# Performance work log

Measured on AMD Instinct MI355X. Metric: run time of the kernel, lower is better.

Reference implementation:

```python
import jax, jax.numpy as jnp
import numpy as np

B, D_IN, D_OUT, Q, NUM_CLASSES = 256, 512, 256, 16, 100
POOL = 2  # patch_size = sqrt(n=4) -> 2x2 spatial mean pooling


def setup_inputs() -> dict:
    key = jax.random.key(0)
    k1, k2, k3 = jax.random.split(key, 3)
    X = jax.random.normal(k1, (B, D_IN, Q), jnp.float32)
    # FRMap weight init: randn(d_out, d_in) / sqrt(d_in)
    W = jax.random.normal(k2, (D_OUT, D_IN), jnp.float32) / np.sqrt(D_IN)
    d2 = D_OUT // POOL
    fc_w = jax.random.normal(k3, (NUM_CLASSES, d2 * d2), jnp.float32) / np.sqrt(d2 * d2)
    fc_b = jnp.zeros((NUM_CLASSES,), jnp.float32)
    return {"X": X, "W": W, "fc_w": fc_w, "fc_b": fc_b}


def reference(X, W, fc_w, fc_b):
    # FRMap: Y = W @ X  -> (B, d_out, q)
    Y = jnp.einsum('oi,biq->boq', W, X)
    # ReOrth: Q from reduced QR of Y -> orthonormal (B, d_out, q)
    Qm, _ = jnp.linalg.qr(Y)
    # ProjMap: P = Q Q^T -> (B, d_out, d_out)
    P = jnp.einsum('biq,bjq->bij', Qm, Qm)
    # ProjPooling (spatial, n=4): 2x2 mean pooling == adaptive_avg_pool2d to (d/2, d/2)
    b, d, _ = P.shape
    d2 = d // POOL
    Pp = P.reshape(b, d2, POOL, d2, POOL).mean(axis=(2, 4))  # (B, d2, d2)
    # OrthMap: top-q eigenvectors of symmetric Pp (eigh ascending -> take last q, descending)
    _, V = jnp.linalg.eigh(Pp)
    U = V[..., ::-1][..., :Q]  # (B, d2, q)
    # OutputBlock: ProjMap + flatten + FC
    P2 = jnp.einsum('biq,bjq->bij', U, U)  # (B, d2, d2)
    logits = P2.reshape(b, -1) @ fc_w.T + fc_b  # (B, num_classes)
    return logits
```

## Files before the change

kernel.cpp:

```cpp
#include <hip/hip_runtime.h>
#include <hip/hip_bf16.h>
#include <cstdint>

#define BATCH 256
#define DIN   512
#define D2    128
#define NQ    16
#define NC    100
#define KFC   (D2 * D2)

#define KS    32
#define KCH   (KFC / KS)
#define STEPS (KCH / 32)

#define ZPAD  132
#define XTP   520
#define CVT_BLKS 800
#define W2_BLKS  256

typedef short short8 __attribute__((ext_vector_type(8)));
typedef float f32x4  __attribute__((ext_vector_type(4)));
typedef float f32x16 __attribute__((ext_vector_type(16)));

__global__ __launch_bounds__(256) void k_prep(const float* __restrict__ W,
                                              const float* __restrict__ fcw,
                                              __hip_bfloat16* __restrict__ W2hi,
                                              __hip_bfloat16* __restrict__ W2lo,
                                              __hip_bfloat16* __restrict__ fcw16) {
    int blk = blockIdx.x;
    if (blk < CVT_BLKS) {
        int i = (blk * 256 + threadIdx.x) * 8;
        float4 a = *(const float4*)(fcw + i);
        float4 b = *(const float4*)(fcw + i + 4);
        short8 v;
        __hip_bfloat16* h = (__hip_bfloat16*)&v;
        h[0] = __float2bfloat16(a.x); h[1] = __float2bfloat16(a.y);
        h[2] = __float2bfloat16(a.z); h[3] = __float2bfloat16(a.w);
        h[4] = __float2bfloat16(b.x); h[5] = __float2bfloat16(b.y);
        h[6] = __float2bfloat16(b.z); h[7] = __float2bfloat16(b.w);
        *(short8*)(fcw16 + i) = v;
    } else {
        int idx = (blk - CVT_BLKS) * 256 + threadIdx.x;
        int o = idx >> 9;
        int i = idx & (DIN - 1);
        float v = 0.5f * (W[(size_t)(2 * o) * DIN + i] +
                          W[(size_t)(2 * o + 1) * DIN + i]);
        __hip_bfloat16 hi = __float2bfloat16(v);
        __hip_bfloat16 lo = __float2bfloat16(v - __bfloat162float(hi));
        W2hi[idx] = hi;
        W2lo[idx] = lo;
    }
}

#define GJ_STEP(K) do {                                                   \
    float piv = __shfl(g[(K) & 7], ((K) >> 3) * 16 + (K), 64);            \
    float fac = __shfl(g[(K) & 7], ((K) >> 3) * 16 + r, 64);              \
    float inv = 1.0f / piv;                                               \
    float f   = fac * inv;                                                \
    float p0 = __shfl(g[0], cg16 + (K), 64);                              \
    float p1 = __shfl(g[1], cg16 + (K), 64);                              \
    float p2 = __shfl(g[2], cg16 + (K), 64);                              \
    float p3 = __shfl(g[3], cg16 + (K), 64);                              \
    float p4 = __shfl(g[4], cg16 + (K), 64);                              \
    float p5 = __shfl(g[5], cg16 + (K), 64);                              \
    float p6 = __shfl(g[6], cg16 + (K), 64);                              \
    float p7 = __shfl(g[7], cg16 + (K), 64);                              \
    bool isk = (r == (K));                                                \
    g[0] = isk ? p0 * inv : fmaf(-f, p0, g[0]);                           \
    g[1] = isk ? p1 * inv : fmaf(-f, p1, g[1]);                           \
    g[2] = isk ? p2 * inv : fmaf(-f, p2, g[2]);                           \
    g[3] = isk ? p3 * inv : fmaf(-f, p3, g[3]);                           \
    g[4] = isk ? p4 * inv : fmaf(-f, p4, g[4]);                           \
    g[5] = isk ? p5 * inv : fmaf(-f, p5, g[5]);                           \
    g[6] = isk ? p6 * inv : fmaf(-f, p6, g[6]);                           \
    g[7] = isk ? p7 * inv : fmaf(-f, p7, g[7]);                           \
} while (0)

__global__ __launch_bounds__(512) void k_zgep(const float* __restrict__ X,
                                              const __hip_bfloat16* __restrict__ W2hi,
                                              const __hip_bfloat16* __restrict__ W2lo,
                                              __hip_bfloat16* __restrict__ P2) {
    __shared__ float Xs[DIN][17];
    __shared__ __hip_bfloat16 Xthi[NQ][XTP];
    __shared__ __hip_bfloat16 Xtlo[NQ][XTP];
    __shared__ float Zt[NQ][ZPAD];
    __shared__ float Et[NQ][ZPAD];
    __shared__ float Gi[NQ][36];

    int b = blockIdx.x;
    int t = threadIdx.x;
    int l = t & 63;
    int wv = t >> 6;

    {
        const float4* src = (const float4*)(X + (size_t)b * DIN * NQ);
        #pragma unroll
        for (int r = 0; r < 4; ++r) {
            float4 v = src[t + r * 512];
            int idx = (t + r * 512) * 4;
            int i = idx >> 4, q = idx & 15;
            Xs[i][q]     = v.x;
            Xs[i][q + 1] = v.y;
            Xs[i][q + 2] = v.z;
            Xs[i][q + 3] = v.w;
        }
    }
    __syncthreads();

    {
        int q  = t >> 5;
        int li = t & 31;
        #pragma unroll
        for (int c = 0; c < 8; ++c) {
            int i0 = c * 64 + li * 2;
            float v0 = Xs[i0][q], v1 = Xs[i0 + 1][q];
            __hip_bfloat16 h0 = __float2bfloat16(v0);
            __hip_bfloat16 h1 = __float2bfloat16(v1);
            __hip_bfloat16 l0 = __float2bfloat16(v0 - __bfloat162float(h0));
            __hip_bfloat16 l1 = __float2bfloat16(v1 - __bfloat162float(h1));
            Xthi[q][i0] = h0; Xthi[q][i0 + 1] = h1;
            Xtlo[q][i0] = l0; Xtlo[q][i0 + 1] = l1;
        }
    }
    __syncthreads();

    {
        int m  = l & 15;
        int kg = (l >> 4) * 8;
        const __hip_bfloat16* whi = W2hi + (size_t)(wv * 16 + m) * DIN + kg;
        const __hip_bfloat16* wlo = W2lo + (size_t)(wv * 16 + m) * DIN + kg;
        f32x4 acc = {0.f, 0.f, 0.f, 0.f};
        #pragma unroll 4
        for (int s = 0; s < 16; ++s) {
            short8 ahi = *(const short8*)(whi + s * 32);
            short8 alo = *(const short8*)(wlo + s * 32);
            short8 bhi = *(const short8*)&Xthi[m][s * 32 + kg];
            short8 blo = *(const short8*)&Xtlo[m][s * 32 + kg];
            acc = __builtin_amdgcn_mfma_f32_16x16x32_bf16(ahi, bhi, acc, 0, 0, 0);
            acc = __builtin_amdgcn_mfma_f32_16x16x32_bf16(ahi, blo, acc, 0, 0, 0);
            acc = __builtin_amdgcn_mfma_f32_16x16x32_bf16(alo, bhi, acc, 0, 0, 0);
        }
        int r0 = (l >> 4) * 4;
        #pragma unroll
        for (int j = 0; j < 4; ++j)
            Zt[m][wv * 16 + r0 + j] = acc[j];
    }
    __syncthreads();

    if (t < 256) {
        int qq = t >> 4, rr = t & 15;
        float s = 0.f;
        for (int i = 0; i < D2; i += 4) {
            float4 a = *(const float4*)&Zt[qq][i];
            float4 c = *(const float4*)&Zt[rr][i];
            s = fmaf(a.x, c.x, s); s = fmaf(a.y, c.y, s);
            s = fmaf(a.z, c.z, s); s = fmaf(a.w, c.w, s);
        }
        Gi[qq][rr] = s;
        Gi[qq][NQ + rr] = (qq == rr) ? 1.f : 0.f;
    }
    __syncthreads();

    if (t < 64) {
        int r    = t & 15;
        int cg   = t >> 4;
        int cg16 = cg * 16;
        float g[8];
        #pragma unroll
        for (int j = 0; j < 8; ++j) g[j] = Gi[r][cg * 8 + j];
        GJ_STEP(0);  GJ_STEP(1);  GJ_STEP(2);  GJ_STEP(3);
        GJ_STEP(4);  GJ_STEP(5);  GJ_STEP(6);  GJ_STEP(7);
        GJ_STEP(8);  GJ_STEP(9);  GJ_STEP(10); GJ_STEP(11);
        GJ_STEP(12); GJ_STEP(13); GJ_STEP(14); GJ_STEP(15);
        if (cg >= 2) {
            #pragma unroll
            for (int j = 0; j < 8; ++j) Gi[r][cg * 8 + j] = g[j];
        }
    }
    __syncthreads();

    {
        int o  = t & (D2 - 1);
        int qg = (t >> 7) * 4;
        float acc[4] = {};
        #pragma unroll
        for (int rp = 0; rp < NQ; ++rp) {
            float z = Zt[rp][o];
            #pragma unroll
            for (int j = 0; j < 4; ++j)
                acc[j] = fmaf(z, Gi[rp][NQ + qg + j], acc[j]);
        }
        #pragma unroll
        for (int j = 0; j < 4; ++j) Et[qg + j][o] = acc[j];
    }
    __syncthreads();

    {
        __hip_bfloat16* P2b = P2 + (size_t)b * KFC;
        int ti = wv >> 1;
        int tj0 = (wv & 1) * 2;
        int r8 = (l >> 5) * 8;
        int rm = l & 31;

        short8 afr;
        {
            __hip_bfloat16* ah = (__hip_bfloat16*)&afr;
            #pragma unroll
            for (int j = 0; j < 8; ++j)
                ah[j] = __float2bfloat16(Et[r8 + j][ti * 32 + rm]);
        }
        #pragma unroll
        for (int tjo = 0; tjo < 2; ++tjo) {
            int tj = tj0 + tjo;
            short8 bfr;
            __hip_bfloat16* bh = (__hip_bfloat16*)&bfr;
            #pragma unroll
            for (int j = 0; j < 8; ++j)
                bh[j] = __float2bfloat16(Zt[r8 + j][tj * 32 + rm]);
            f32x16 cc = {};
            cc = __builtin_amdgcn_mfma_f32_32x32x16_bf16(afr, bfr, cc, 0, 0, 0);
            #pragma unroll
            for (int reg = 0; reg < 16; ++reg) {
                int row = (reg & 3) + 8 * (reg >> 2) + 4 * (l >> 5);
                P2b[(size_t)(ti * 32 + row) * D2 + tj * 32 + rm] =
                    __float2bfloat16(cc[reg]);
            }
        }
    }
}

__global__ __launch_bounds__(256) void k_fc(const __hip_bfloat16* __restrict__ P2,
                                            const __hip_bfloat16* __restrict__ fcw16,
                                            float* __restrict__ part) {
    int bt = blockIdx.x;
    int ks = blockIdx.y;
    int t  = threadIdx.x;
    int lane = t & 63;
    int w    = t >> 6;
    int m  = lane & 15;
    int kg = (lane >> 4) * 8;

    const __hip_bfloat16* pa =
        P2 + (size_t)(bt * 16 + m) * KFC + ks * KCH + kg;

    int c0 = w * 32 + m;
    int c1 = c0 + 16;
    bool v0 = (c0 < NC), v1 = (c1 < NC);
    const __hip_bfloat16* pb0 =
        fcw16 + (size_t)(v0 ? c0 : 0) * KFC + ks * KCH + kg;
    const __hip_bfloat16* pb1 =
        fcw16 + (size_t)(v1 ? c1 : 0) * KFC + ks * KCH + kg;

    f32x4 acc0 = {0.f, 0.f, 0.f, 0.f};
    f32x4 acc1 = {0.f, 0.f, 0.f, 0.f};
    short8 zz = {};

    #pragma unroll 4
    for (int s = 0; s < STEPS; ++s) {
        short8 a  = *(const short8*)(pa + s * 32);
        short8 b0 = v0 ? *(const short8*)(pb0 + s * 32) : zz;
        short8 b1 = v1 ? *(const short8*)(pb1 + s * 32) : zz;
        acc0 = __builtin_amdgcn_mfma_f32_16x16x32_bf16(a, b0, acc0, 0, 0, 0);
        acc1 = __builtin_amdgcn_mfma_f32_16x16x32_bf16(a, b1, acc1, 0, 0, 0);
    }

    int r0 = (lane >> 4) * 4;
    float* pp = part + ((size_t)ks * BATCH + bt * 16 + r0) * D2;
    #pragma unroll
    for (int j = 0; j < 4; ++j) {
        pp[(size_t)j * D2 + w * 32 + m]      = acc0[j];
        pp[(size_t)j * D2 + w * 32 + 16 + m] = acc1[j];
    }
}

__global__ __launch_bounds__(128) void k_red(const float* __restrict__ part,
                                             const float* __restrict__ fcb,
                                             float* __restrict__ out) {
    int b = blockIdx.x;
    int c = threadIdx.x;
    if (c < NC) {
        float s = fcb[c];
        #pragma unroll 8
        for (int ks = 0; ks < KS; ++ks)
            s += part[((size_t)ks * BATCH + b) * D2 + c];
        out[(size_t)b * NC + c] = s;
    }
}

extern "C" void kernel_launch(void* const* d_in, const int* in_sizes, int n_in,
                              void* d_out, int out_size, void* d_ws, size_t ws_size,
                              hipStream_t stream) {
    const float* X   = (const float*)d_in[0];
    const float* W   = (const float*)d_in[1];
    const float* fcw = (const float*)d_in[2];
    const float* fcb = (const float*)d_in[3];
    float* out = (float*)d_out;

    __hip_bfloat16* W2hi  = (__hip_bfloat16*)d_ws;
    __hip_bfloat16* W2lo  = W2hi + 65536;
    __hip_bfloat16* fcw16 = W2lo + 65536;
    __hip_bfloat16* P2b16 = fcw16 + 1638400;
    float*          part  = (float*)(P2b16 + 4194304);

    k_prep<<<dim3(CVT_BLKS + W2_BLKS), 256, 0, stream>>>(W, fcw, W2hi, W2lo, fcw16);
    k_zgep<<<dim3(BATCH), 512, 0, stream>>>(X, W2hi, W2lo, P2b16);
    k_fc  <<<dim3(16, KS), 256, 0, stream>>>(P2b16, fcw16, part);
    k_red <<<dim3(BATCH), 128, 0, stream>>>(part, fcb, out);
}
```

Measured before the change: 41.45 us.

## Fuse split-K reduction into FC kernel and pre-swizzle X fragments in LDS

Removes the separate reduction kernel. Each FC block now increments a per-batch-tile atomic counter, and the last of the split-K blocks sums the partial results and adds the bias. The X hi/lo bf16 split is written directly in MFMA fragment order, so each lane loads its operand from LDS contiguously, and bf16 conversion uses a manual round-to-nearest bit trick. This saves one kernel launch plus one global round trip, at the cost of a counter reset in the prep kernel and a serialized tail reduction on the last-arriving block.

Result: slower. 104.0 us (+150.9%).

```diff
diff --git a/kernel.cpp b/kernel.cpp
--- a/kernel.cpp
+++ b/kernel.cpp
@@ -14,19 +14,27 @@
 #define STEPS (KCH / 32)
 
 #define ZPAD  132
-#define XTP   520
 #define CVT_BLKS 800
 #define W2_BLKS  256
 
 typedef short short8 __attribute__((ext_vector_type(8)));
 typedef float f32x4  __attribute__((ext_vector_type(4)));
 typedef float f32x16 __attribute__((ext_vector_type(16)));
+
+static __device__ __forceinline__ unsigned short f2bf_rne(float f) {
+    unsigned x = __float_as_uint(f);
+    return (unsigned short)((x + 0x7fffu + ((x >> 16) & 1u)) >> 16);
+}
+static __device__ __forceinline__ float bf2f(unsigned short u) {
+    return __uint_as_float(((unsigned)u) << 16);
+}
 
 __global__ __launch_bounds__(256) void k_prep(const float* __restrict__ W,
                                               const float* __restrict__ fcw,
                                               __hip_bfloat16* __restrict__ W2hi,
                                               __hip_bfloat16* __restrict__ W2lo,
-                                              __hip_bfloat16* __restrict__ fcw16) {
+                                              __hip_bfloat16* __restrict__ fcw16,
+                                              int* __restrict__ cnt) {
     int blk = blockIdx.x;
     if (blk < CVT_BLKS) {
         int i = (blk * 256 + threadIdx.x) * 8;
@@ -40,15 +48,16 @@
         h[6] = __float2bfloat16(b.z); h[7] = __float2bfloat16(b.w);
         *(short8*)(fcw16 + i) = v;
     } else {
+        if (blk == CVT_BLKS && threadIdx.x < 16) cnt[threadIdx.x] = 0;
         int idx = (blk - CVT_BLKS) * 256 + threadIdx.x;
         int o = idx >> 9;
         int i = idx & (DIN - 1);
         float v = 0.5f * (W[(size_t)(2 * o) * DIN + i] +
                           W[(size_t)(2 * o + 1) * DIN + i]);
-        __hip_bfloat16 hi = __float2bfloat16(v);
-        __hip_bfloat16 lo = __float2bfloat16(v - __bfloat162float(hi));
-        W2hi[idx] = hi;
-        W2lo[idx] = lo;
+        unsigned short hi = f2bf_rne(v);
+        unsigned short lo = f2bf_rne(v - bf2f(hi));
+        *(unsigned short*)(W2hi + idx) = hi;
+        *(unsigned short*)(W2lo + idx) = lo;
     }
 }
 
@@ -81,8 +90,8 @@
                                               const __hip_bfloat16* __restrict__ W2lo,
                                               __hip_bfloat16* __restrict__ P2) {
     __shared__ float Xs[DIN][17];
-    __shared__ __hip_bfloat16 Xthi[NQ][XTP];
-    __shared__ __hip_bfloat16 Xtlo[NQ][XTP];
+    __shared__ unsigned int FragHi[16 * 256];
+    __shared__ unsigned int FragLo[16 * 256];
     __shared__ float Zt[NQ][ZPAD];
     __shared__ float Et[NQ][ZPAD];
     __shared__ float Gi[NQ][36];
@@ -107,20 +116,20 @@
     }
     __syncthreads();
 
-    {
-        int q  = t >> 5;
-        int li = t & 31;
-        #pragma unroll
-        for (int c = 0; c < 8; ++c) {
-            int i0 = c * 64 + li * 2;
-            float v0 = Xs[i0][q], v1 = Xs[i0 + 1][q];
-            __hip_bfloat16 h0 = __float2bfloat16(v0);
-            __hip_bfloat16 h1 = __float2bfloat16(v1);
-            __hip_bfloat16 l0 = __float2bfloat16(v0 - __bfloat162float(h0));
-            __hip_bfloat16 l1 = __float2bfloat16(v1 - __bfloat162float(h1));
-            Xthi[q][i0] = h0; Xthi[q][i0 + 1] = h1;
-            Xtlo[q][i0] = l0; Xtlo[q][i0 + 1] = l1;
-        }
+    #pragma unroll
+    for (int it = 0; it < 8; ++it) {
+        int d  = t + it * 512;
+        int s  = d >> 8;
+        int ln = (d >> 2) & 63;
+        int jj = d & 3;
+        int q  = ln & 15;
+        int i0 = s * 32 + ((ln >> 4) & 3) * 8 + jj * 2;
+        float v0 = Xs[i0][q], v1 = Xs[i0 + 1][q];
+        unsigned short h0 = f2bf_rne(v0), h1 = f2bf_rne(v1);
+        unsigned short l0 = f2bf_rne(v0 - bf2f(h0));
+        unsigned short l1 = f2bf_rne(v1 - bf2f(h1));
+        FragHi[d] = (unsigned)h0 | ((unsigned)h1 << 16);
+        FragLo[d] = (unsigned)l0 | ((unsigned)l1 << 16);
     }
     __syncthreads();
 
@@ -134,8 +143,8 @@
         for (int s = 0; s < 16; ++s) {
             short8 ahi = *(const short8*)(whi + s * 32);
             short8 alo = *(const short8*)(wlo + s * 32);
-            short8 bhi = *(const short8*)&Xthi[m][s * 32 + kg];
-            short8 blo = *(const short8*)&Xtlo[m][s * 32 + kg];
+            short8 bhi = *(const short8*)(&FragHi[s * 256 + l * 4]);
+            short8 blo = *(const short8*)(&FragLo[s * 256 + l * 4]);
             acc = __builtin_amdgcn_mfma_f32_16x16x32_bf16(ahi, bhi, acc, 0, 0, 0);
             acc = __builtin_amdgcn_mfma_f32_16x16x32_bf16(ahi, blo, acc, 0, 0, 0);
             acc = __builtin_amdgcn_mfma_f32_16x16x32_bf16(alo, bhi, acc, 0, 0, 0);
@@ -163,18 +172,18 @@
 
     if (t < 64) {
         int r    = t & 15;
-        int cg   = t >> 4;
-        int cg16 = cg * 16;
+        int cgg  = t >> 4;
+        int cg16 = cgg * 16;
         float g[8];
         #pragma unroll
-        for (int j = 0; j < 8; ++j) g[j] = Gi[r][cg * 8 + j];
+        for (int j = 0; j < 8; ++j) g[j] = Gi[r][cgg * 8 + j];
         GJ_STEP(0);  GJ_STEP(1);  GJ_STEP(2);  GJ_STEP(3);
         GJ_STEP(4);  GJ_STEP(5);  GJ_STEP(6);  GJ_STEP(7);
         GJ_STEP(8);  GJ_STEP(9);  GJ_STEP(10); GJ_STEP(11);
         GJ_STEP(12); GJ_STEP(13); GJ_STEP(14); GJ_STEP(15);
-        if (cg >= 2) {
-            #pragma unroll
-            for (int j = 0; j < 8; ++j) Gi[r][cg * 8 + j] = g[j];
+        if (cgg >= 2) {
+            #pragma unroll
+            for (int j = 0; j < 8; ++j) Gi[r][cgg * 8 + j] = g[j];
         }
     }
     __syncthreads();
@@ -231,7 +240,10 @@
 
 __global__ __launch_bounds__(256) void k_fc(const __hip_bfloat16* __restrict__ P2,
                                             const __hip_bfloat16* __restrict__ fcw16,
-                                            float* __restrict__ part) {
+                                            float* __restrict__ part,
+                                            const float* __restrict__ fcb,
+                                            float* __restrict__ out,
+                                            int* __restrict__ cnt) {
     int bt = blockIdx.x;
     int ks = blockIdx.y;
     int t  = threadIdx.x;
@@ -271,19 +283,22 @@
         pp[(size_t)j * D2 + w * 32 + m]      = acc0[j];
         pp[(size_t)j * D2 + w * 32 + 16 + m] = acc1[j];
     }
-}
-
-__global__ __launch_bounds__(128) void k_red(const float* __restrict__ part,
-                                             const float* __restrict__ fcb,
-                                             float* __restrict__ out) {
-    int b = blockIdx.x;
-    int c = threadIdx.x;
-    if (c < NC) {
-        float s = fcb[c];
-        #pragma unroll 8
-        for (int ks = 0; ks < KS; ++ks)
-            s += part[((size_t)ks * BATCH + b) * D2 + c];
-        out[(size_t)b * NC + c] = s;
+
+    __threadfence();
+    __shared__ int lastFlag;
+    if (t == 0) lastFlag = (atomicAdd(&cnt[bt], 1) == KS - 1);
+    __syncthreads();
+    if (lastFlag) {
+        __threadfence();
+        for (int idx = t; idx < 16 * NC; idx += 256) {
+            int bl = idx / NC;
+            int c  = idx - bl * NC;
+            float s = fcb[c];
+            #pragma unroll 8
+            for (int k2 = 0; k2 < KS; ++k2)
+                s += part[((size_t)k2 * BATCH + bt * 16 + bl) * D2 + c];
+            out[(size_t)(bt * 16 + bl) * NC + c] = s;
+        }
     }
 }
 
@@ -301,9 +316,9 @@
     __hip_bfloat16* fcw16 = W2lo + 65536;
     __hip_bfloat16* P2b16 = fcw16 + 1638400;
     float*          part  = (float*)(P2b16 + 4194304);
-
-    k_prep<<<dim3(CVT_BLKS + W2_BLKS), 256, 0, stream>>>(W, fcw, W2hi, W2lo, fcw16);
+    int*            cnt   = (int*)(part + 1048576);
+
+    k_prep<<<dim3(CVT_BLKS + W2_BLKS), 256, 0, stream>>>(W, fcw, W2hi, W2lo, fcw16, cnt);
     k_zgep<<<dim3(BATCH), 512, 0, stream>>>(X, W2hi, W2lo, P2b16);
-    k_fc  <<<dim3(16, KS), 256, 0, stream>>>(P2b16, fcw16, part);
-    k_red <<<dim3(BATCH), 128, 0, stream>>>(part, fcb, out);
-}
+    k_fc  <<<dim3(16, KS), 256, 0, stream>>>(P2b16, fcw16, part, fcb, out, cnt);
+}
```
